# Kernel optimization log

Hardware: AMD Instinct MI355X
Metric: run time of the kernel (lower is better)

The kernel has to match this reference:

```python
import jax, jax.numpy as jnp
import numpy as np

B, N, D, E, H, HS = 2, 1024, 256, 64, 8, 64
FF = 4 * D
EPS = 1e-6


def _glorot(key, shape):
    fan_in, fan_out = shape[-2], shape[-1]
    lim = np.sqrt(6.0 / (fan_in + fan_out))
    return jax.random.uniform(key, shape, jnp.float32, -lim, lim)


def setup_inputs() -> dict:
    key = jax.random.key(0)
    ks = jax.random.split(key, 10)
    return {
        "node": jax.random.normal(ks[0], (B, N, D), jnp.float32),
        "edge": jax.random.normal(ks[1], (B, N, N, E), jnp.float32),
        "Wq": _glorot(ks[2], (H, D, HS)),
        "Wk": _glorot(ks[3], (H, D + E, HS)),
        "Wv": _glorot(ks[4], (H, D, HS)),
        "Wp": _glorot(ks[5], (H, HS, D)),
        "bp": jnp.zeros((D,), jnp.float32),
        "ln1_g": jnp.ones((D,), jnp.float32),
        "ln1_b": jnp.zeros((D,), jnp.float32),
        "W1": _glorot(ks[6], (D, FF)),
        "b1": jnp.zeros((FF,), jnp.float32),
        "W2": _glorot(ks[7], (FF, D)),
        "b2": jnp.zeros((D,), jnp.float32),
        "ln2_g": jnp.ones((D,), jnp.float32),
        "ln2_b": jnp.zeros((D,), jnp.float32),
    }


def _layernorm(x, g, b):
    mu = jnp.mean(x, axis=-1, keepdims=True)
    var = jnp.mean(jnp.square(x - mu), axis=-1, keepdims=True)
    return (x - mu) * jax.lax.rsqrt(var + EPS) * g + b


def reference(node, edge, Wq, Wk, Wv, Wp, bp, ln1_g, ln1_b, W1, b1, W2, b2, ln2_g, ln2_b):
    d_in = node.shape[-1]
    head_size = Wq.shape[-1]
    # query projection, scaled by sqrt(head_size)
    q = jnp.einsum('bni,hio->bnho', node, Wq) / jnp.sqrt(jnp.asarray(head_size, node.dtype))
    # key kernel split: node part [H, D, HS] and edge part [H, E, HS].
    # concat([repeat(key), edge]) @ Wk  ==  key @ Wk[:, :D] + edge @ Wk[:, D:]
    kn = jnp.einsum('bmi,hio->bmho', node, Wk[:, :d_in])          # [B,M,H,HS]
    logits = jnp.einsum('bnho,bmho->bhnm', q, kn)                 # node-key logits
    qe = jnp.einsum('bnho,heo->bnhe', q, Wk[:, d_in:])            # [B,N,H,E]
    logits = logits + jnp.einsum('bnhe,bnme->bhnm', qe, edge)     # edge-conditioned logits
    attn = jax.nn.softmax(logits, axis=-1)                        # [B,H,N,M]
    v = jnp.einsum('bmi,hio->bmho', node, Wv)                     # [B,M,H,HS]
    mo = jnp.einsum('bhnm,bmho->bnho', attn, v)                   # [B,N,H,HS]
    mha = jnp.einsum('bnhi,hio->bno', mo, Wp) + bp                # output projection
    # residual + layernorm (dropout = identity at eval)
    x = _layernorm(node + mha, ln1_g, ln1_b)
    # FFN: one hidden layer of ff_multi*D with relu, then project back to D
    ff = jax.nn.relu(x @ W1 + b1) @ W2 + b2
    return _layernorm(x + ff, ln2_g, ln2_b)
```

## Files before the change

### kernel.cpp

```cpp
#include <hip/hip_runtime.h>
#include <hip/hip_bf16.h>
#include <hip/hip_fp16.h>

#define B_  2
#define N_  1024
#define D_  256
#define E_  64
#define H_  8
#define HS_ 64
#define FF_ 1024
#define R_  (B_*N_)

typedef short bf8 __attribute__((ext_vector_type(8)));
typedef float f4  __attribute__((ext_vector_type(4)));

static __device__ __forceinline__ ushort f2b(float f) {
  __hip_bfloat16 h = __float2bfloat16(f);
  return *reinterpret_cast<ushort*>(&h);
}

static __device__ __forceinline__ ushort4 f4_to_b4(float4 v) {
  ushort4 r;
  r.x = f2b(v.x); r.y = f2b(v.y); r.z = f2b(v.z); r.w = f2b(v.w);
  return r;
}

__global__ void k_pack(const float* __restrict__ node, const float* __restrict__ Wq,
                       const float* __restrict__ Wk, const float* __restrict__ Wv,
                       const float* __restrict__ Wp, const float* __restrict__ W1,
                       const float* __restrict__ W2,
                       ushort* __restrict__ node_bf, ushort* __restrict__ wqkvT,
                       ushort* __restrict__ wkeT, ushort* __restrict__ wpT,
                       ushort* __restrict__ w1T, ushort* __restrict__ w2T) {
  int idx = blockIdx.x * 256 + threadIdx.x;
  if (idx < 524288) {
    node_bf[idx] = f2b(node[idx]);
    return;
  }
  idx -= 524288;
  if (idx < 393216) {
    int c = idx >> 8, i = idx & 255;
    int mat = c >> 9, h = (c >> 6) & 7, o = c & 63;
    float v;
    if (mat == 0)      v = Wq[(h * 256 + i) * 64 + o] * 0.125f;
    else if (mat == 1) v = Wk[(h * 320 + i) * 64 + o];
    else               v = Wv[(h * 256 + i) * 64 + o];
    wqkvT[idx] = f2b(v);
    return;
  }
  idx -= 393216;
  if (idx < 262144) {
    int c = idx >> 9, r = idx & 511;
    int h2 = c >> 6, e = c & 63, h = r >> 6, o = r & 63;
    wkeT[idx] = (h2 == h) ? f2b(Wk[(h * 320 + 256 + e) * 64 + o]) : (ushort)0;
    return;
  }
  idx -= 262144;
  if (idx < 131072) {
    int c = idx >> 9, r = idx & 511;
    wpT[idx] = f2b(Wp[r * 256 + c]);
    return;
  }
  idx -= 131072;
  if (idx < 262144) {
    int c = idx >> 8, k = idx & 255;
    w1T[idx] = f2b(W1[k * 1024 + c]);
    return;
  }
  idx -= 262144;
  {
    int c = idx >> 10, k = idx & 1023;
    w2T[idx] = f2b(W2[k * 256 + c]);
  }
}

__global__ void k_vT(const ushort* __restrict__ qkv, ushort* __restrict__ vt) {
  int idx = blockIdx.x * 256 + threadIdx.x;
  if (idx >= 16 * 64 * 1024) return;
  int m = idx & 1023;
  int rest = idx >> 10;
  int o = rest & 63;
  int bh = rest >> 6;
  int b = bh >> 3, h = bh & 7;
  vt[idx] = qkv[(size_t)(b * 1024 + m) * 1536 + 1024 + h * 64 + o];
}

template<int EPI, int OFMT>
__global__ void k_gemm(const ushort* __restrict__ A, const ushort* __restrict__ Bt,
                       void* __restrict__ Cv, const float* __restrict__ bias,
                       int M, int N, int K, int lda, int ldbt, int ldc,
                       long long as1, long long as2, long long bs1, long long bs2,
                       long long cs1, long long cs2) {
  int z = blockIdx.z;
  const ushort* Ab = A  + (size_t)((z >> 3) * as1 + (z & 7) * as2);
  const ushort* Bb = Bt + (size_t)((z >> 3) * bs1 + (z & 7) * bs2);
  size_t coff = (size_t)((z >> 3) * cs1 + (z & 7) * cs2);
  int r0 = blockIdx.x * 64, c0 = blockIdx.y * 64;

  __shared__ ushort As[64][40];
  __shared__ ushort Bs[64][40];

  int tid = threadIdx.x;
  int lane = tid & 63, w = tid >> 6;
  int wm = w >> 1, wn = w & 1;
  int kg = lane >> 4, lr = lane & 15;

  f4 acc[2][2] = {};

  for (int k0 = 0; k0 < K; k0 += 32) {
    __syncthreads();
    {
      int row = tid >> 2, ch = tid & 3;
      *(int4*)&As[row][ch * 8] = *(const int4*)(Ab + (size_t)(r0 + row) * lda + k0 + ch * 8);
    }
    {
      int row = tid >> 2, ch = tid & 3;
      *(int4*)&Bs[row][ch * 8] = *(const int4*)(Bb + (size_t)(c0 + row) * ldbt + k0 + ch * 8);
    }
    __syncthreads();

    bf8 bfr[2];
    #pragma unroll
    for (int cb = 0; cb < 2; ++cb)
      bfr[cb] = *(const bf8*)&Bs[wn * 32 + cb * 16 + lr][kg * 8];
    #pragma unroll
    for (int rb = 0; rb < 2; ++rb) {
      bf8 af = *(const bf8*)&As[wm * 32 + rb * 16 + lr][kg * 8];
      #pragma unroll
      for (int cb = 0; cb < 2; ++cb)
        acc[rb][cb] = __builtin_amdgcn_mfma_f32_16x16x32_bf16(af, bfr[cb], acc[rb][cb], 0, 0, 0);
    }
  }

  float*  Cf = (float*)Cv;
  ushort* Cb = (ushort*)Cv;
  __half* Ch = (__half*)Cv;
  #pragma unroll
  for (int rb = 0; rb < 2; ++rb) {
    #pragma unroll
    for (int cb = 0; cb < 2; ++cb) {
      #pragma unroll
      for (int rr = 0; rr < 4; ++rr) {
        int row = r0 + wm * 32 + rb * 16 + kg * 4 + rr;
        int col = c0 + wn * 32 + cb * 16 + lr;
        size_t ci = coff + (size_t)row * ldc + col;
        float v = acc[rb][cb][rr];
        if (EPI >= 2) v += bias[col];
        if (EPI == 3) v = fmaxf(v, 0.0f);
        if (OFMT == 1)      Cb[ci] = f2b(v);
        else if (OFMT == 2) Ch[ci] = __float2half(v);
        else                Cf[ci] = v;
      }
    }
  }
}

__global__ __launch_bounds__(256, 4) void k_fused(
    const float* __restrict__ edge, const float* __restrict__ qe,
    const __half* __restrict__ logN, ushort* __restrict__ attn) {
  int bid = blockIdx.x;
  int b = bid >> 10, n = bid & 1023;
  int t = threadIdx.x;
  int lane = t & 63, w = t >> 6;
  int kg = lane >> 4, lr = lane & 15;

  __shared__ ushort As[128 * 64];
  __shared__ __half lg[1024 * 9];
  __shared__ float red[2][4][8];

  bf8 bq[2];
  {
    const float* qrow = qe + (size_t)bid * 512 + (size_t)(lr & 7) * 64;
    #pragma unroll
    for (int kk = 0; kk < 2; ++kk) {
      float4 a  = *reinterpret_cast<const float4*>(&qrow[kk * 32 + kg * 8]);
      float4 c4 = *reinterpret_cast<const float4*>(&qrow[kk * 32 + kg * 8 + 4]);
      bq[kk][0] = (short)f2b(a.x);  bq[kk][1] = (short)f2b(a.y);
      bq[kk][2] = (short)f2b(a.z);  bq[kk][3] = (short)f2b(a.w);
      bq[kk][4] = (short)f2b(c4.x); bq[kk][5] = (short)f2b(c4.y);
      bq[kk][6] = (short)f2b(c4.z); bq[kk][7] = (short)f2b(c4.w);
    }
  }

  const float* eb = edge + (size_t)bid * 65536;

  float4 pf[8];
  #pragma unroll
  for (int u = 0; u < 8; ++u)
    pf[u] = reinterpret_cast<const float4*>(eb)[t + 256 * u];

  #pragma unroll 1
  for (int tl = 0; tl < 8; ++tl) {
    __syncthreads();
    #pragma unroll
    for (int u = 0; u < 8; ++u) {
      int g = t + 256 * u;
      int rl = g >> 4, c = t & 15;
      int slot = (c >> 1) ^ (rl & 7), half = c & 1;
      *reinterpret_cast<ushort4*>(&As[rl * 64 + slot * 8 + half * 4]) = f4_to_b4(pf[u]);
    }
    if (tl < 7) {
      const float4* src = reinterpret_cast<const float4*>(eb + (tl + 1) * 8192);
      #pragma unroll
      for (int u = 0; u < 8; ++u) pf[u] = src[t + 256 * u];
    }
    __syncthreads();

    #pragma unroll
    for (int sub = 0; sub < 2; ++sub) {
      int sr = w * 32 + sub * 16 + lr;
      f4 acc = {};
      #pragma unroll
      for (int kk = 0; kk < 2; ++kk) {
        bf8 af = *reinterpret_cast<const bf8*>(&As[sr * 64 + (((kk * 4 + kg) ^ (sr & 7)) << 3)]);
        acc = __builtin_amdgcn_mfma_f32_16x16x32_bf16(af, bq[kk], acc, 0, 0, 0);
      }
      if (lr < 8) {
        int mbase = tl * 128 + w * 32 + sub * 16 + kg * 4;
        #pragma unroll
        for (int rr = 0; rr < 4; ++rr)
          lg[(mbase + rr) * 9 + lr] = __float2half(acc[rr]);
      }
    }
  }
  __syncthreads();

  float l[4][8];
  #pragma unroll
  for (int j = 0; j < 4; ++j) {
    int m = t + 256 * j;
    #pragma unroll
    for (int h = 0; h < 8; ++h)
      l[j][h] = __half2float(lg[m * 9 + h]) +
                __half2float(logN[((size_t)(b * 8 + h) * 1024 + n) * 1024 + m]);
  }
  float mx[8], sm[8];
  #pragma unroll
  for (int h = 0; h < 8; ++h) {
    float v = fmaxf(fmaxf(l[0][h], l[1][h]), fmaxf(l[2][h], l[3][h]));
    #pragma unroll
    for (int off = 32; off; off >>= 1) v = fmaxf(v, __shfl_xor(v, off));
    if (lane == 0) red[0][w][h] = v;
  }
  __syncthreads();
  #pragma unroll
  for (int h = 0; h < 8; ++h)
    mx[h] = fmaxf(fmaxf(red[0][0][h], red[0][1][h]), fmaxf(red[0][2][h], red[0][3][h]));
  #pragma unroll
  for (int j = 0; j < 4; ++j)
    #pragma unroll
    for (int h = 0; h < 8; ++h)
      l[j][h] = __expf(l[j][h] - mx[h]);
  #pragma unroll
  for (int h = 0; h < 8; ++h) {
    float v = l[0][h] + l[1][h] + l[2][h] + l[3][h];
    #pragma unroll
    for (int off = 32; off; off >>= 1) v += __shfl_xor(v, off);
    if (lane == 0) red[1][w][h] = v;
  }
  __syncthreads();
  #pragma unroll
  for (int h = 0; h < 8; ++h)
    sm[h] = 1.0f / (red[1][0][h] + red[1][1][h] + red[1][2][h] + red[1][3][h]);
  #pragma unroll
  for (int h = 0; h < 8; ++h) {
    size_t base = ((size_t)(b * 8 + h) * 1024 + n) * 1024;
    #pragma unroll
    for (int j = 0; j < 4; ++j)
      attn[base + t + 256 * j] = f2b(l[j][h] * sm[h]);
  }
}

__global__ void k_ln(const float* __restrict__ a, const float* __restrict__ bb,
                     const float* __restrict__ g, const float* __restrict__ be,
                     float* __restrict__ of, ushort* __restrict__ ob) {
  int r = blockIdx.x, i = threadIdx.x;
  float t = a[(size_t)r * 256 + i] + bb[(size_t)r * 256 + i];
  __shared__ float red[4];

  float s = t;
  for (int off = 32; off; off >>= 1) s += __shfl_xor(s, off);
  if ((i & 63) == 0) red[i >> 6] = s;
  __syncthreads();
  float mean = (red[0] + red[1] + red[2] + red[3]) * (1.0f / 256.0f);
  __syncthreads();

  float d = t - mean;
  float q = d * d;
  for (int off = 32; off; off >>= 1) q += __shfl_xor(q, off);
  if ((i & 63) == 0) red[i >> 6] = q;
  __syncthreads();
  float var = (red[0] + red[1] + red[2] + red[3]) * (1.0f / 256.0f);

  float y = d * rsqrtf(var + 1e-6f) * g[i] + be[i];
  of[(size_t)r * 256 + i] = y;
  if (ob) ob[(size_t)r * 256 + i] = f2b(y);
}


extern "C" void kernel_launch(void* const* d_in, const int* in_sizes, int n_in,
                              void* d_out, int out_size, void* d_ws, size_t ws_size,
                              hipStream_t stream) {
  (void)in_sizes; (void)n_in; (void)out_size; (void)ws_size;
  const float* node = (const float*)d_in[0];
  const float* edge = (const float*)d_in[1];
  const float* Wq   = (const float*)d_in[2];
  const float* Wk   = (const float*)d_in[3];
  const float* Wv   = (const float*)d_in[4];
  const float* Wp   = (const float*)d_in[5];
  const float* bp   = (const float*)d_in[6];
  const float* g1   = (const float*)d_in[7];
  const float* be1  = (const float*)d_in[8];
  const float* W1   = (const float*)d_in[9];
  const float* b1   = (const float*)d_in[10];
  const float* W2   = (const float*)d_in[11];
  const float* b2   = (const float*)d_in[12];
  const float* g2   = (const float*)d_in[13];
  const float* be2  = (const float*)d_in[14];
  float* out = (float*)d_out;

  char* ws = (char*)d_ws;
  size_t off = 0;
  auto alloc = [&](size_t bytes) -> char* {
    char* p = ws + off;
    off = (off + bytes + 255) & ~(size_t)255;
    return p;
  };
  ushort* node_bf = (ushort*)alloc((size_t)R_ * D_ * 2);
  ushort* wqkvT   = (ushort*)alloc((size_t)1536 * 256 * 2);
  ushort* wkeT    = (ushort*)alloc((size_t)512 * 512 * 2);
  ushort* wpT     = (ushort*)alloc((size_t)256 * 512 * 2);
  ushort* w1T     = (ushort*)alloc((size_t)1024 * 256 * 2);
  ushort* w2T     = (ushort*)alloc((size_t)256 * 1024 * 2);
  ushort* qkv     = (ushort*)alloc((size_t)R_ * 1536 * 2);
  float*  qe      = (float*) alloc((size_t)R_ * 512 * 4);
  ushort* vt      = (ushort*)alloc((size_t)16 * 64 * 1024 * 2);
  __half* logits  = (__half*)alloc((size_t)16 * 1024 * 1024 * 2);
  ushort* attn    = (ushort*)alloc((size_t)16 * 1024 * 1024 * 2);
  ushort* mo      = (ushort*)alloc((size_t)R_ * 512 * 2);
  float*  mha     = (float*) alloc((size_t)R_ * 256 * 4);
  float*  xf      = (float*) alloc((size_t)R_ * 256 * 4);
  ushort* xb      = (ushort*)alloc((size_t)R_ * 256 * 2);
  ushort* hb      = (ushort*)alloc((size_t)R_ * 1024 * 2);
  float*  ff      = (float*) alloc((size_t)R_ * 256 * 4);

  k_pack<<<dim3(7168), dim3(256), 0, stream>>>(node, Wq, Wk, Wv, Wp, W1, W2,
                                               node_bf, wqkvT, wkeT, wpT, w1T, w2T);

  k_gemm<0, 1><<<dim3(32, 24, 1), dim3(256), 0, stream>>>(
      node_bf, wqkvT, qkv, nullptr, 2048, 1536, 256, 256, 256, 1536,
      0LL, 0LL, 0LL, 0LL, 0LL, 0LL);

  k_gemm<0, 0><<<dim3(32, 8, 1), dim3(256), 0, stream>>>(
      qkv, wkeT, qe, nullptr, 2048, 512, 512, 1536, 512, 512,
      0LL, 0LL, 0LL, 0LL, 0LL, 0LL);

  k_vT<<<dim3(4096), dim3(256), 0, stream>>>(qkv, vt);

  k_gemm<0, 2><<<dim3(16, 16, 16), dim3(256), 0, stream>>>(
      qkv, qkv + 512, logits, nullptr, 1024, 1024, 64, 1536, 1536, 1024,
      1572864LL, 64LL, 1572864LL, 64LL, 8388608LL, 1048576LL);

  k_fused<<<dim3(2048), dim3(256), 0, stream>>>(edge, qe, logits, attn);

  k_gemm<0, 1><<<dim3(16, 1, 16), dim3(256), 0, stream>>>(
      attn, vt, mo, nullptr, 1024, 64, 1024, 1024, 1024, 512,
      8388608LL, 1048576LL, 524288LL, 65536LL, 524288LL, 64LL);

  k_gemm<2, 0><<<dim3(32, 4, 1), dim3(256), 0, stream>>>(
      mo, wpT, mha, bp, 2048, 256, 512, 512, 512, 256,
      0LL, 0LL, 0LL, 0LL, 0LL, 0LL);

  k_ln<<<dim3(2048), dim3(256), 0, stream>>>(node, mha, g1, be1, xf, xb);

  k_gemm<3, 1><<<dim3(32, 16, 1), dim3(256), 0, stream>>>(
      xb, w1T, hb, b1, 2048, 1024, 256, 256, 256, 1024,
      0LL, 0LL, 0LL, 0LL, 0LL, 0LL);

  k_gemm<2, 0><<<dim3(32, 4, 1), dim3(256), 0, stream>>>(
      hb, w2T, ff, b2, 2048, 256, 1024, 1024, 1024, 256,
      0LL, 0LL, 0LL, 0LL, 0LL, 0LL);

  k_ln<<<dim3(2048), dim3(256), 0, stream>>>(xf, ff, g2, be2, out, nullptr);
}
```

Before: 231.6 us.

## Fuse output-proj and FFN2 GEMMs with layernorm, widen logits tiles, skip zero blocks

Adds a k_gemm_ln kernel where each block computes a full 64x256 output row tile and applies bias, residual and layernorm in registers. It replaces the separate Wp/W2 GEMMs and the two layernorm kernels, removing the mha and ff buffers and two launches. The logits GEMM now computes four 64-column B tiles per block, and the qe GEMM only iterates over its diagonal K block, which assumes the packed wkeT is block-diagonal. The logN prefetch in k_fused is also hoisted before the barrier. Risks: the fused LN kernels launch only 32 blocks, which is low occupancy on a large GPU, and the diagonal skip depends on the weight layout.

```diff
diff --git a/kernel.cpp b/kernel.cpp
--- a/kernel.cpp
+++ b/kernel.cpp
@@ -85,7 +85,7 @@
   vt[idx] = qkv[(size_t)(b * 1024 + m) * 1536 + 1024 + h * 64 + o];
 }
 
-template<int EPI, int OFMT>
+template<int EPI, int OFMT, int NBT, bool BDIAG>
 __global__ void k_gemm(const ushort* __restrict__ A, const ushort* __restrict__ Bt,
                        void* __restrict__ Cv, const float* __restrict__ bias,
                        int M, int N, int K, int lda, int ldbt, int ldc,
@@ -95,40 +95,45 @@
   const ushort* Ab = A  + (size_t)((z >> 3) * as1 + (z & 7) * as2);
   const ushort* Bb = Bt + (size_t)((z >> 3) * bs1 + (z & 7) * bs2);
   size_t coff = (size_t)((z >> 3) * cs1 + (z & 7) * cs2);
-  int r0 = blockIdx.x * 64, c0 = blockIdx.y * 64;
+  int r0 = blockIdx.x * 64, c0 = blockIdx.y * (64 * NBT);
 
   __shared__ ushort As[64][40];
-  __shared__ ushort Bs[64][40];
+  __shared__ ushort Bs[64 * NBT][40];
 
   int tid = threadIdx.x;
   int lane = tid & 63, w = tid >> 6;
   int wm = w >> 1, wn = w & 1;
   int kg = lane >> 4, lr = lane & 15;
 
-  f4 acc[2][2] = {};
-
-  for (int k0 = 0; k0 < K; k0 += 32) {
+  f4 acc[2][2 * NBT] = {};
+
+  int kbeg = BDIAG ? c0 : 0;
+  int kend = BDIAG ? c0 + 64 : K;
+  for (int k0 = kbeg; k0 < kend; k0 += 32) {
     __syncthreads();
     {
       int row = tid >> 2, ch = tid & 3;
       *(int4*)&As[row][ch * 8] = *(const int4*)(Ab + (size_t)(r0 + row) * lda + k0 + ch * 8);
     }
-    {
-      int row = tid >> 2, ch = tid & 3;
+    #pragma unroll
+    for (int i = 0; i < NBT; ++i) {
+      int row = (tid >> 2) + 64 * i, ch = tid & 3;
       *(int4*)&Bs[row][ch * 8] = *(const int4*)(Bb + (size_t)(c0 + row) * ldbt + k0 + ch * 8);
     }
     __syncthreads();
 
-    bf8 bfr[2];
-    #pragma unroll
-    for (int cb = 0; cb < 2; ++cb)
-      bfr[cb] = *(const bf8*)&Bs[wn * 32 + cb * 16 + lr][kg * 8];
+    bf8 bfr[2 * NBT];
+    #pragma unroll
+    for (int nt = 0; nt < NBT; ++nt)
+      #pragma unroll
+      for (int cb = 0; cb < 2; ++cb)
+        bfr[nt * 2 + cb] = *(const bf8*)&Bs[nt * 64 + wn * 32 + cb * 16 + lr][kg * 8];
     #pragma unroll
     for (int rb = 0; rb < 2; ++rb) {
       bf8 af = *(const bf8*)&As[wm * 32 + rb * 16 + lr][kg * 8];
       #pragma unroll
-      for (int cb = 0; cb < 2; ++cb)
-        acc[rb][cb] = __builtin_amdgcn_mfma_f32_16x16x32_bf16(af, bfr[cb], acc[rb][cb], 0, 0, 0);
+      for (int q = 0; q < 2 * NBT; ++q)
+        acc[rb][q] = __builtin_amdgcn_mfma_f32_16x16x32_bf16(af, bfr[q], acc[rb][q], 0, 0, 0);
     }
   }
 
@@ -138,19 +143,88 @@
   #pragma unroll
   for (int rb = 0; rb < 2; ++rb) {
     #pragma unroll
-    for (int cb = 0; cb < 2; ++cb) {
+    for (int q = 0; q < 2 * NBT; ++q) {
       #pragma unroll
       for (int rr = 0; rr < 4; ++rr) {
         int row = r0 + wm * 32 + rb * 16 + kg * 4 + rr;
-        int col = c0 + wn * 32 + cb * 16 + lr;
+        int col = c0 + (q >> 1) * 64 + wn * 32 + (q & 1) * 16 + lr;
         size_t ci = coff + (size_t)row * ldc + col;
-        float v = acc[rb][cb][rr];
+        float v = acc[rb][q][rr];
         if (EPI >= 2) v += bias[col];
         if (EPI == 3) v = fmaxf(v, 0.0f);
         if (OFMT == 1)      Cb[ci] = f2b(v);
         else if (OFMT == 2) Ch[ci] = __float2half(v);
         else                Cf[ci] = v;
       }
+    }
+  }
+}
+
+__global__ __launch_bounds__(256) void k_gemm_ln(
+    const ushort* __restrict__ A, const ushort* __restrict__ Bt,
+    const float* __restrict__ bias, const float* __restrict__ resid,
+    const float* __restrict__ g, const float* __restrict__ be,
+    float* __restrict__ of, ushort* __restrict__ ob, int K) {
+  int r0 = blockIdx.x * 64;
+  __shared__ ushort As[64][40];
+  __shared__ ushort Bs[256][40];
+  int tid = threadIdx.x, lane = tid & 63, w = tid >> 6;
+  int kg = lane >> 4, lr = lane & 15;
+
+  f4 acc[16] = {};
+  for (int k0 = 0; k0 < K; k0 += 32) {
+    __syncthreads();
+    { int row = tid >> 2, ch = tid & 3;
+      *(int4*)&As[row][ch * 8] = *(const int4*)(A + (size_t)(r0 + row) * K + k0 + ch * 8); }
+    #pragma unroll
+    for (int j = 0; j < 4; ++j) {
+      int pos = tid + 256 * j, row = pos >> 2, ch = pos & 3;
+      *(int4*)&Bs[row][ch * 8] = *(const int4*)(Bt + (size_t)row * K + k0 + ch * 8);
+    }
+    __syncthreads();
+    bf8 af = *(const bf8*)&As[w * 16 + lr][kg * 8];
+    #pragma unroll
+    for (int fc = 0; fc < 16; ++fc) {
+      bf8 bf = *(const bf8*)&Bs[fc * 16 + lr][kg * 8];
+      acc[fc] = __builtin_amdgcn_mfma_f32_16x16x32_bf16(af, bf, acc[fc], 0, 0, 0);
+    }
+  }
+
+  #pragma unroll
+  for (int fc = 0; fc < 16; ++fc) {
+    int col = fc * 16 + lr;
+    #pragma unroll
+    for (int rr = 0; rr < 4; ++rr) {
+      int row = r0 + w * 16 + kg * 4 + rr;
+      acc[fc][rr] += bias[col] + resid[(size_t)row * 256 + col];
+    }
+  }
+  float mean[4], rstd[4];
+  #pragma unroll
+  for (int rr = 0; rr < 4; ++rr) {
+    float s = 0.f;
+    #pragma unroll
+    for (int fc = 0; fc < 16; ++fc) s += acc[fc][rr];
+    #pragma unroll
+    for (int off = 1; off < 16; off <<= 1) s += __shfl_xor(s, off);
+    mean[rr] = s * (1.0f / 256.0f);
+    float q = 0.f;
+    #pragma unroll
+    for (int fc = 0; fc < 16; ++fc) { float d = acc[fc][rr] - mean[rr]; q += d * d; }
+    #pragma unroll
+    for (int off = 1; off < 16; off <<= 1) q += __shfl_xor(q, off);
+    rstd[rr] = rsqrtf(q * (1.0f / 256.0f) + 1e-6f);
+  }
+  #pragma unroll
+  for (int fc = 0; fc < 16; ++fc) {
+    int col = fc * 16 + lr;
+    float gg = g[col], bb = be[col];
+    #pragma unroll
+    for (int rr = 0; rr < 4; ++rr) {
+      int row = r0 + w * 16 + kg * 4 + rr;
+      float y = (acc[fc][rr] - mean[rr]) * rstd[rr] * gg + bb;
+      of[(size_t)row * 256 + col] = y;
+      if (ob) ob[(size_t)row * 256 + col] = f2b(y);
     }
   }
 }
@@ -223,6 +297,14 @@
       }
     }
   }
+
+  ushort lNr[4][8];
+  #pragma unroll
+  for (int j = 0; j < 4; ++j)
+    #pragma unroll
+    for (int h = 0; h < 8; ++h)
+      lNr[j][h] = *reinterpret_cast<const ushort*>(
+          &logN[((size_t)(b * 8 + h) * 1024 + n) * 1024 + t + 256 * j]);
   __syncthreads();
 
   float l[4][8];
@@ -232,7 +314,7 @@
     #pragma unroll
     for (int h = 0; h < 8; ++h)
       l[j][h] = __half2float(lg[m * 9 + h]) +
-                __half2float(logN[((size_t)(b * 8 + h) * 1024 + n) * 1024 + m]);
+                __half2float(*reinterpret_cast<const __half*>(&lNr[j][h]));
   }
   float mx[8], sm[8];
   #pragma unroll
@@ -269,32 +351,6 @@
     for (int j = 0; j < 4; ++j)
       attn[base + t + 256 * j] = f2b(l[j][h] * sm[h]);
   }
-}
-
-__global__ void k_ln(const float* __restrict__ a, const float* __restrict__ bb,
-                     const float* __restrict__ g, const float* __restrict__ be,
-                     float* __restrict__ of, ushort* __restrict__ ob) {
-  int r = blockIdx.x, i = threadIdx.x;
-  float t = a[(size_t)r * 256 + i] + bb[(size_t)r * 256 + i];
-  __shared__ float red[4];
-
-  float s = t;
-  for (int off = 32; off; off >>= 1) s += __shfl_xor(s, off);
-  if ((i & 63) == 0) red[i >> 6] = s;
-  __syncthreads();
-  float mean = (red[0] + red[1] + red[2] + red[3]) * (1.0f / 256.0f);
-  __syncthreads();
-
-  float d = t - mean;
-  float q = d * d;
-  for (int off = 32; off; off >>= 1) q += __shfl_xor(q, off);
-  if ((i & 63) == 0) red[i >> 6] = q;
-  __syncthreads();
-  float var = (red[0] + red[1] + red[2] + red[3]) * (1.0f / 256.0f);
-
-  float y = d * rsqrtf(var + 1e-6f) * g[i] + be[i];
-  of[(size_t)r * 256 + i] = y;
-  if (ob) ob[(size_t)r * 256 + i] = f2b(y);
 }
 
 
@@ -338,48 +394,40 @@
   __half* logits  = (__half*)alloc((size_t)16 * 1024 * 1024 * 2);
   ushort* attn    = (ushort*)alloc((size_t)16 * 1024 * 1024 * 2);
   ushort* mo      = (ushort*)alloc((size_t)R_ * 512 * 2);
-  float*  mha     = (float*) alloc((size_t)R_ * 256 * 4);
   float*  xf      = (float*) alloc((size_t)R_ * 256 * 4);
   ushort* xb      = (ushort*)alloc((size_t)R_ * 256 * 2);
   ushort* hb      = (ushort*)alloc((size_t)R_ * 1024 * 2);
-  float*  ff      = (float*) alloc((size_t)R_ * 256 * 4);
 
   k_pack<<<dim3(7168), dim3(256), 0, stream>>>(node, Wq, Wk, Wv, Wp, W1, W2,
                                                node_bf, wqkvT, wkeT, wpT, w1T, w2T);
 
-  k_gemm<0, 1><<<dim3(32, 24, 1), dim3(256), 0, stream>>>(
+  k_gemm<0, 1, 1, false><<<dim3(32, 24, 1), dim3(256), 0, stream>>>(
       node_bf, wqkvT, qkv, nullptr, 2048, 1536, 256, 256, 256, 1536,
       0LL, 0LL, 0LL, 0LL, 0LL, 0LL);
 
-  k_gemm<0, 0><<<dim3(32, 8, 1), dim3(256), 0, stream>>>(
+  k_gemm<0, 0, 1, true><<<dim3(32, 8, 1), dim3(256), 0, stream>>>(
       qkv, wkeT, qe, nullptr, 2048, 512, 512, 1536, 512, 512,
       0LL, 0LL, 0LL, 0LL, 0LL, 0LL);
 
   k_vT<<<dim3(4096), dim3(256), 0, stream>>>(qkv, vt);
 
-  k_gemm<0, 2><<<dim3(16, 16, 16), dim3(256), 0, stream>>>(
+  k_gemm<0, 2, 4, false><<<dim3(16, 4, 16), dim3(256), 0, stream>>>(
       qkv, qkv + 512, logits, nullptr, 1024, 1024, 64, 1536, 1536, 1024,
       1572864LL, 64LL, 1572864LL, 64LL, 8388608LL, 1048576LL);
 
   k_fused<<<dim3(2048), dim3(256), 0, stream>>>(edge, qe, logits, attn);
 
-  k_gemm<0, 1><<<dim3(16, 1, 16), dim3(256), 0, stream>>>(
+  k_gemm<0, 1, 1, false><<<dim3(16, 1, 16), dim3(256), 0, stream>>>(
       attn, vt, mo, nullptr, 1024, 64, 1024, 1024, 1024, 512,
       8388608LL, 1048576LL, 524288LL, 65536LL, 524288LL, 64LL);
 
-  k_gemm<2, 0><<<dim3(32, 4, 1), dim3(256), 0, stream>>>(
-      mo, wpT, mha, bp, 2048, 256, 512, 512, 512, 256,
-      0LL, 0LL, 0LL, 0LL, 0LL, 0LL);
-
-  k_ln<<<dim3(2048), dim3(256), 0, stream>>>(node, mha, g1, be1, xf, xb);
-
-  k_gemm<3, 1><<<dim3(32, 16, 1), dim3(256), 0, stream>>>(
+  k_gemm_ln<<<dim3(32), dim3(256), 0, stream>>>(
+      mo, wpT, bp, node, g1, be1, xf, xb, 512);
+
+  k_gemm<3, 1, 1, false><<<dim3(32, 16, 1), dim3(256), 0, stream>>>(
       xb, w1T, hb, b1, 2048, 1024, 256, 256, 256, 1024,
       0LL, 0LL, 0LL, 0LL, 0LL, 0LL);
 
-  k_gemm<2, 0><<<dim3(32, 4, 1), dim3(256), 0, stream>>>(
-      hb, w2T, ff, b2, 2048, 256, 1024, 1024, 1024, 256,
-      0LL, 0LL, 0LL, 0LL, 0LL, 0LL);
-
-  k_ln<<<dim3(2048), dim3(256), 0, stream>>>(xf, ff, g2, be2, out, nullptr);
-}
+  k_gemm_ln<<<dim3(32), dim3(256), 0, stream>>>(
+      hb, w2T, b2, xf, g2, be2, out, nullptr, 1024);
+}
```

New measurement: 250.2 us. +8.0%, slower.
